# Performance work log

Measured on AMD Instinct MI355X. Metric: run time of the kernel, lower is better.

The kernel has to match this reference:

```python
import jax, jax.numpy as jnp
import numpy as np

B = 4096           # number of paths
N_STEPS = 4        # module hops per path (3 with tanh + final without)
E = 128            # embed_size
NUM_AUTHOR = 500000
NUM_MODULE = 64
OUT_DIM = 16       # classifier_output_dim


def setup_inputs() -> dict:
    key = jax.random.key(0)
    ks = jax.random.split(key, 7)
    author_ids = jax.random.randint(ks[0], (B,), 0, NUM_AUTHOR)
    module_ids = jax.random.randint(ks[1], (B, N_STEPS), 0, NUM_MODULE)
    # learned parameters (torch nn.Embedding / nn.Linear layout: W is [out, in])
    embed_table = jax.random.normal(ks[2], (NUM_AUTHOR, E), dtype=jnp.float32)
    W = jax.random.normal(ks[3], (NUM_MODULE, E, E), dtype=jnp.float32) * (1.0 / np.sqrt(E))
    b = jax.random.normal(ks[4], (NUM_MODULE, E), dtype=jnp.float32) * 0.01
    cls_W = jax.random.normal(ks[5], (OUT_DIM, E), dtype=jnp.float32) * (1.0 / np.sqrt(E))
    cls_b = jax.random.normal(ks[6], (OUT_DIM,), dtype=jnp.float32) * 0.01
    return {"author_ids": author_ids, "module_ids": module_ids,
            "embed_table": embed_table, "W": W, "b": b,
            "cls_W": cls_W, "cls_b": cls_b}


def reference(author_ids, module_ids, embed_table, W, b, cls_W, cls_b):
    # x = author embedding lookup (path[0])           [B, E]
    x = embed_table[author_ids]
    n_steps = module_ids.shape[1]
    # dynamically-selected Linear+tanh chain; final Linear has no tanh
    for i in range(n_steps):
        ids = module_ids[:, i]                        # [B]
        Wi = W[ids]                                   # [B, E, E] (out, in)
        bi = b[ids]                                   # [B, E]
        y = jnp.einsum('bi,boi->bo', x, Wi) + bi
        x = jnp.tanh(y) if i < n_steps - 1 else y
    # classifier: Linear(E -> OUT_DIM)
    return x @ cls_W.T + cls_b
```

## Files before the change

kernel.cpp:

```cpp
#include <hip/hip_runtime.h>

#define B_TOT   4096
#define NSTEPS  4
#define E       128
#define OUT_DIM 16
#define NMOD    64
#define KSPLIT  8
#define TILE    16

using frag8 = __attribute__((ext_vector_type(8))) short;
using f32x4 = __attribute__((ext_vector_type(4))) float;

__device__ __forceinline__ unsigned short f2bf(float x) {
    union { float f; unsigned u; } v; v.f = x;
    unsigned r = v.u + 0x7FFFu + ((v.u >> 16) & 1u);
    return (unsigned short)(r >> 16);
}
__device__ __forceinline__ float bf2f(unsigned short h) {
    union { unsigned u; float f; } v; v.u = ((unsigned)h) << 16;
    return v.f;
}
__device__ __forceinline__ unsigned pack2(unsigned short a, unsigned short b) {
    return (unsigned)a | ((unsigned)b << 16);
}
__device__ __forceinline__ float tanh_fast(float x) {
    return 1.0f - 2.0f / (__expf(2.0f * x) + 1.0f);
}


__global__ __launch_bounds__(1024) void sort_kernel(const int* __restrict__ mids,
                                                    int* __restrict__ ws)
{
    const int s = blockIdx.x;
    const int t = threadIdx.x;
    __shared__ int h[NMOD];
    __shared__ int o[NMOD];
    if (t < NMOD) h[t] = 0;
    __syncthreads();
    for (int b = t; b < B_TOT; b += 1024)
        atomicAdd(&h[mids[b * NSTEPS + s]], 1);
    __syncthreads();
    if (t == 0) {
        int run = 0;
        for (int m = 0; m < NMOD; ++m) { o[m] = run; run += h[m]; }
    }
    __syncthreads();
    if (t < NMOD) {
        ws[s * NMOD + t]       = h[t];
        ws[256 + s * NMOD + t] = o[t];
        h[t] = o[t];
    }
    __syncthreads();
    int* perm = ws + 512 + s * B_TOT;
    for (int b = t; b < B_TOT; b += 1024) {
        const int m = mids[b * NSTEPS + s];
        const int p = atomicAdd(&h[m], 1);
        perm[p] = b;
    }
}

template <bool FIRST, bool LAST>
__global__ __launch_bounds__(256) void step_kernel(
    const int s,
    const int* __restrict__ ws,
    const int* __restrict__ author_ids,
    const float* __restrict__ embed,
    const float* __restrict__ W,
    const float* __restrict__ bias,
    const float* __restrict__ cls_W,
    const float* __restrict__ cls_b,
    float* __restrict__ xbuf,
    float* __restrict__ out)
{
    const int m = blockIdx.x >> 3;
    const int k = blockIdx.x & (KSPLIT - 1);
    const int cnt = ws[s * NMOD + m];
    const int off = ws[256 + s * NMOD + m];
    const int start = off + k * TILE;
    const int end   = off + cnt;
    if (start >= end) return;

    const int t  = threadIdx.x;
    const int w  = t >> 6;
    const int l  = t & 63;
    const int g  = l >> 4;
    const int r0 = l & 15;

    __shared__ __align__(16) unsigned short Whi[E * E];
    __shared__ __align__(16) unsigned short Wlo[E * E];
    __shared__ __align__(16) unsigned short Xhi[TILE * E];
    __shared__ __align__(16) unsigned short Xlo[TILE * E];
    __shared__ __align__(16) float bl[E];
    __shared__ int rowb[TILE];
    __shared__ __align__(16) float YlS[LAST ? TILE * (E + 4) : 1];
    __shared__ __align__(16) float cwlS[LAST ? OUT_DIM * (E + 4) : 1];

    {
        const f32x4* __restrict__ wg = (const f32x4*)(W + (size_t)m * E * E);
        #pragma unroll
        for (int i = 0; i < 16; ++i) {
            const f32x4 v = wg[i * 256 + t];
            const int f  = (i * 256 + t) * 4;
            const int c  = f >> 7;
            const int kk = f & 127;
            const int idx = c * E + (((kk >> 3) ^ (c & 15)) << 3) + (kk & 7);
            const unsigned short h0 = f2bf(v.x), h1 = f2bf(v.y),
                                 h2 = f2bf(v.z), h3 = f2bf(v.w);
            const unsigned short q0 = f2bf(v.x - bf2f(h0)), q1 = f2bf(v.y - bf2f(h1)),
                                 q2 = f2bf(v.z - bf2f(h2)), q3 = f2bf(v.w - bf2f(h3));
            uint2 hp = { pack2(h0, h1), pack2(h2, h3) };
            uint2 lp = { pack2(q0, q1), pack2(q2, q3) };
            *(uint2*)&Whi[idx] = hp;
            *(uint2*)&Wlo[idx] = lp;
        }
        if (t < 32)
            ((f32x4*)bl)[t] = ((const f32x4*)(bias + m * E))[t];
        if (LAST) {
            #pragma unroll
            for (int i = 0; i < 2; ++i) {
                const int fi = i * 256 + t;
                const f32x4 v = ((const f32x4*)cls_W)[fi];
                const int j  = (fi * 4) >> 7;
                const int kk = (fi * 4) & 127;
                *(f32x4*)&cwlS[j * (E + 4) + kk] = v;
            }
        }
    }

    const int* __restrict__ perm = ws + 512 + s * B_TOT;
    const int c0 = 32 * w + r0;
    const int c1 = c0 + 16;

    for (int base = start; base < end; base += KSPLIT * TILE) {
        const int nb = min(TILE, end - base);

        {
            const int row = t >> 4, u0 = t & 15;
            f32x4 v0 = {0.f, 0.f, 0.f, 0.f}, v1 = {0.f, 0.f, 0.f, 0.f};
            if (row < nb) {
                const int b = perm[base + row];
                if (u0 == 0) rowb[row] = b;
                const float* __restrict__ src =
                    FIRST ? (embed + (size_t)author_ids[b] * E)
                          : (xbuf + (size_t)b * E);
                v0 = ((const f32x4*)src)[u0 * 2];
                v1 = ((const f32x4*)src)[u0 * 2 + 1];
            }
            const float xf[8] = {v0.x, v0.y, v0.z, v0.w, v1.x, v1.y, v1.z, v1.w};
            unsigned short hh[8], qq[8];
            #pragma unroll
            for (int j = 0; j < 8; ++j) {
                hh[j] = f2bf(xf[j]);
                qq[j] = f2bf(xf[j] - bf2f(hh[j]));
            }
            const int idx = row * E + ((u0 ^ row) << 3);
            uint4 hp = { pack2(hh[0], hh[1]), pack2(hh[2], hh[3]),
                         pack2(hh[4], hh[5]), pack2(hh[6], hh[7]) };
            uint4 lp = { pack2(qq[0], qq[1]), pack2(qq[2], qq[3]),
                         pack2(qq[4], qq[5]), pack2(qq[6], qq[7]) };
            *(uint4*)&Xhi[idx] = hp;
            *(uint4*)&Xlo[idx] = lp;
        }
        __syncthreads();

        frag8 ahi[4], alo[4];
        #pragma unroll
        for (int ss = 0; ss < 4; ++ss) {
            const int idx = r0 * E + (((4 * ss + g) ^ r0) << 3);
            ahi[ss] = *(const frag8*)&Xhi[idx];
            alo[ss] = *(const frag8*)&Xlo[idx];
        }

        f32x4 acc0 = {0.f, 0.f, 0.f, 0.f};
        f32x4 acc1 = {0.f, 0.f, 0.f, 0.f};
        #pragma unroll
        for (int ss = 0; ss < 4; ++ss) {
            const int u = ((4 * ss + g) ^ r0) << 3;
            {
                const int idx = c0 * E + u;
                const frag8 bh = *(const frag8*)&Whi[idx];
                const frag8 bq = *(const frag8*)&Wlo[idx];
                acc0 = __builtin_amdgcn_mfma_f32_16x16x32_bf16(ahi[ss], bh, acc0, 0, 0, 0);
                acc0 = __builtin_amdgcn_mfma_f32_16x16x32_bf16(alo[ss], bh, acc0, 0, 0, 0);
                acc0 = __builtin_amdgcn_mfma_f32_16x16x32_bf16(ahi[ss], bq, acc0, 0, 0, 0);
            }
            {
                const int idx = c1 * E + u;
                const frag8 bh = *(const frag8*)&Whi[idx];
                const frag8 bq = *(const frag8*)&Wlo[idx];
                acc1 = __builtin_amdgcn_mfma_f32_16x16x32_bf16(ahi[ss], bh, acc1, 0, 0, 0);
                acc1 = __builtin_amdgcn_mfma_f32_16x16x32_bf16(alo[ss], bh, acc1, 0, 0, 0);
                acc1 = __builtin_amdgcn_mfma_f32_16x16x32_bf16(ahi[ss], bq, acc1, 0, 0, 0);
            }
        }

        if (!LAST) {
            const float b0 = bl[c0], b1 = bl[c1];
            #pragma unroll
            for (int r = 0; r < 4; ++r) {
                const int row = 4 * g + r;
                if (row < nb) {
                    float* __restrict__ dst = xbuf + (size_t)rowb[row] * E;
                    dst[c0] = tanh_fast(acc0[r] + b0);
                    dst[c1] = tanh_fast(acc1[r] + b1);
                }
            }
            __syncthreads();
        } else {
            const float b0 = bl[c0], b1 = bl[c1];
            #pragma unroll
            for (int r = 0; r < 4; ++r) {
                const int row = 4 * g + r;
                YlS[row * (E + 4) + c0] = acc0[r] + b0;
                YlS[row * (E + 4) + c1] = acc1[r] + b1;
            }
            __syncthreads();
            const int row = t >> 4, j = t & 15;
            if (row < nb) {
                float a2 = cls_b[j];
                #pragma unroll 8
                for (int jj = 0; jj < 32; ++jj) {
                    const f32x4 y4 = *(const f32x4*)&YlS[row * (E + 4) + jj * 4];
                    const f32x4 w4 = *(const f32x4*)&cwlS[j * (E + 4) + jj * 4];
                    a2 += y4.x * w4.x + y4.y * w4.y + y4.z * w4.z + y4.w * w4.w;
                }
                out[(size_t)rowb[row] * OUT_DIM + j] = a2;
            }
            __syncthreads();
        }
    }
}

extern "C" void kernel_launch(void* const* d_in, const int* in_sizes, int n_in,
                              void* d_out, int out_size, void* d_ws, size_t ws_size,
                              hipStream_t stream) {
    const int*   author_ids = (const int*)d_in[0];
    const int*   module_ids = (const int*)d_in[1];
    const float* embed      = (const float*)d_in[2];
    const float* W          = (const float*)d_in[3];
    const float* bias       = (const float*)d_in[4];
    const float* cls_W      = (const float*)d_in[5];
    const float* cls_b      = (const float*)d_in[6];
    float* out = (float*)d_out;

    int*   wsI  = (int*)d_ws;
    float* xbuf = (float*)((char*)d_ws + (512 + NSTEPS * B_TOT) * sizeof(int));

    sort_kernel<<<NSTEPS, 1024, 0, stream>>>(module_ids, wsI);

    const dim3 g(NMOD * KSPLIT), blk(256);
    step_kernel<true,  false><<<g, blk, 0, stream>>>(0, wsI, author_ids, embed, W, bias, cls_W, cls_b, xbuf, out);
    step_kernel<false, false><<<g, blk, 0, stream>>>(1, wsI, author_ids, embed, W, bias, cls_W, cls_b, xbuf, out);
    step_kernel<false, false><<<g, blk, 0, stream>>>(2, wsI, author_ids, embed, W, bias, cls_W, cls_b, xbuf, out);
    step_kernel<false, true ><<<g, blk, 0, stream>>>(3, wsI, author_ids, embed, W, bias, cls_W, cls_b, xbuf, out);
}
```

Baseline: 48.14 us.

## Precompute bf16 hi/lo weight fragments once and drop LDS staging in step kernels

Result: slower. 50.14 us (+4.1%).

```diff
diff --git a/kernel.cpp b/kernel.cpp
--- a/kernel.cpp
+++ b/kernel.cpp
@@ -8,6 +8,9 @@
 #define KSPLIT  8
 #define TILE    16
 
+#define XBUF_BYTE  67584
+#define WFRAG_BYTE 2164736
+
 using frag8 = __attribute__((ext_vector_type(8))) short;
 using f32x4 = __attribute__((ext_vector_type(4))) float;
 
@@ -23,39 +26,71 @@
 __device__ __forceinline__ unsigned pack2(unsigned short a, unsigned short b) {
     return (unsigned)a | ((unsigned)b << 16);
 }
+__device__ __forceinline__ frag8 u4frag(uint4 u) {
+    union { uint4 u; frag8 f; } v; v.u = u; return v.f;
+}
 __device__ __forceinline__ float tanh_fast(float x) {
     return 1.0f - 2.0f / (__expf(2.0f * x) + 1.0f);
 }
 
-
-__global__ __launch_bounds__(1024) void sort_kernel(const int* __restrict__ mids,
-                                                    int* __restrict__ ws)
+__global__ __launch_bounds__(1024) void prep_sort_kernel(
+    const int* __restrict__ mids, const float* __restrict__ W, int* __restrict__ ws)
 {
-    const int s = blockIdx.x;
     const int t = threadIdx.x;
-    __shared__ int h[NMOD];
-    __shared__ int o[NMOD];
-    if (t < NMOD) h[t] = 0;
-    __syncthreads();
-    for (int b = t; b < B_TOT; b += 1024)
-        atomicAdd(&h[mids[b * NSTEPS + s]], 1);
-    __syncthreads();
-    if (t == 0) {
-        int run = 0;
-        for (int m = 0; m < NMOD; ++m) { o[m] = run; run += h[m]; }
-    }
-    __syncthreads();
-    if (t < NMOD) {
-        ws[s * NMOD + t]       = h[t];
-        ws[256 + s * NMOD + t] = o[t];
-        h[t] = o[t];
-    }
-    __syncthreads();
-    int* perm = ws + 512 + s * B_TOT;
-    for (int b = t; b < B_TOT; b += 1024) {
-        const int m = mids[b * NSTEPS + s];
-        const int p = atomicAdd(&h[m], 1);
-        perm[p] = b;
+    if (blockIdx.x < NSTEPS) {
+        const int s = blockIdx.x;
+        __shared__ int h[NMOD];
+        __shared__ int o[NMOD];
+        if (t < NMOD) h[t] = 0;
+        __syncthreads();
+        for (int b = t; b < B_TOT; b += 1024)
+            atomicAdd(&h[mids[b * NSTEPS + s]], 1);
+        __syncthreads();
+        if (t == 0) {
+            int run = 0;
+            for (int m = 0; m < NMOD; ++m) { o[m] = run; run += h[m]; }
+        }
+        __syncthreads();
+        if (t < NMOD) {
+            ws[s * NMOD + t]       = h[t];
+            ws[256 + s * NMOD + t] = o[t];
+            h[t] = o[t];
+        }
+        __syncthreads();
+        int* perm = ws + 512 + s * B_TOT;
+        for (int b = t; b < B_TOT; b += 1024) {
+            const int m = mids[b * NSTEPS + s];
+            const int p = atomicAdd(&h[m], 1);
+            perm[p] = b;
+        }
+    } else {
+        const int m = blockIdx.x - NSTEPS;
+        uint4* __restrict__ wf = (uint4*)((char*)ws + WFRAG_BYTE);
+        const f32x4* __restrict__ wg = (const f32x4*)(W + (size_t)m * E * E);
+        #pragma unroll
+        for (int i = 0; i < 2; ++i) {
+            const int f  = i * 1024 + t;
+            const int c  = f >> 4;
+            const int ss = (f >> 2) & 3;
+            const int g  = f & 3;
+            const int fi = (c * E + ss * 32 + g * 8) >> 2;
+            const f32x4 v0 = wg[fi];
+            const f32x4 v1 = wg[fi + 1];
+            const float xf[8] = {v0.x, v0.y, v0.z, v0.w, v1.x, v1.y, v1.z, v1.w};
+            unsigned short hh[8], qq[8];
+            #pragma unroll
+            for (int j = 0; j < 8; ++j) {
+                hh[j] = f2bf(xf[j]);
+                qq[j] = f2bf(xf[j] - bf2f(hh[j]));
+            }
+            const uint4 H = { pack2(hh[0], hh[1]), pack2(hh[2], hh[3]),
+                              pack2(hh[4], hh[5]), pack2(hh[6], hh[7]) };
+            const uint4 L = { pack2(qq[0], qq[1]), pack2(qq[2], qq[3]),
+                              pack2(qq[4], qq[5]), pack2(qq[6], qq[7]) };
+            const int u = m * 4096 + ss * 512 + c * 4 + g;
+            wf[u]        = H;
+            wf[u + 2048] = L;
+        }
     }
 }
 
@@ -65,11 +100,9 @@
     const int* __restrict__ ws,
     const int* __restrict__ author_ids,
     const float* __restrict__ embed,
-    const float* __restrict__ W,
     const float* __restrict__ bias,
     const float* __restrict__ cls_W,
     const float* __restrict__ cls_b,
-    float* __restrict__ xbuf,
     float* __restrict__ out)
 {
     const int m = blockIdx.x >> 3;
@@ -85,146 +118,106 @@
     const int l  = t & 63;
     const int g  = l >> 4;
     const int r0 = l & 15;
-
-    __shared__ __align__(16) unsigned short Whi[E * E];
-    __shared__ __align__(16) unsigned short Wlo[E * E];
-    __shared__ __align__(16) unsigned short Xhi[TILE * E];
-    __shared__ __align__(16) unsigned short Xlo[TILE * E];
-    __shared__ __align__(16) float bl[E];
-    __shared__ int rowb[TILE];
-    __shared__ __align__(16) float YlS[LAST ? TILE * (E + 4) : 1];
-    __shared__ __align__(16) float cwlS[LAST ? OUT_DIM * (E + 4) : 1];
-
-    {
-        const f32x4* __restrict__ wg = (const f32x4*)(W + (size_t)m * E * E);
-        #pragma unroll
-        for (int i = 0; i < 16; ++i) {
-            const f32x4 v = wg[i * 256 + t];
-            const int f  = (i * 256 + t) * 4;
-            const int c  = f >> 7;
-            const int kk = f & 127;
-            const int idx = c * E + (((kk >> 3) ^ (c & 15)) << 3) + (kk & 7);
-            const unsigned short h0 = f2bf(v.x), h1 = f2bf(v.y),
-                                 h2 = f2bf(v.z), h3 = f2bf(v.w);
-            const unsigned short q0 = f2bf(v.x - bf2f(h0)), q1 = f2bf(v.y - bf2f(h1)),
-                                 q2 = f2bf(v.z - bf2f(h2)), q3 = f2bf(v.w - bf2f(h3));
-            uint2 hp = { pack2(h0, h1), pack2(h2, h3) };
-            uint2 lp = { pack2(q0, q1), pack2(q2, q3) };
-            *(uint2*)&Whi[idx] = hp;
-            *(uint2*)&Wlo[idx] = lp;
-        }
-        if (t < 32)
-            ((f32x4*)bl)[t] = ((const f32x4*)(bias + m * E))[t];
-        if (LAST) {
-            #pragma unroll
-            for (int i = 0; i < 2; ++i) {
-                const int fi = i * 256 + t;
-                const f32x4 v = ((const f32x4*)cls_W)[fi];
-                const int j  = (fi * 4) >> 7;
-                const int kk = (fi * 4) & 127;
-                *(f32x4*)&cwlS[j * (E + 4) + kk] = v;
-            }
-        }
-    }
-
-    const int* __restrict__ perm = ws + 512 + s * B_TOT;
     const int c0 = 32 * w + r0;
     const int c1 = c0 + 16;
 
+    const int* __restrict__ perm = ws + 512 + s * B_TOT;
+    unsigned* __restrict__ xbufP = (unsigned*)((char*)ws + XBUF_BYTE);
+    const uint4* __restrict__ wf = (const uint4*)((char*)ws + WFRAG_BYTE) + m * 4096;
+
+    const float b0 = bias[m * E + c0];
+    const float b1 = bias[m * E + c1];
+
+    __shared__ __align__(16) float Yl[LAST ? TILE * (E + 4) : 1];
+
     for (int base = start; base < end; base += KSPLIT * TILE) {
         const int nb = min(TILE, end - base);
 
-        {
-            const int row = t >> 4, u0 = t & 15;
-            f32x4 v0 = {0.f, 0.f, 0.f, 0.f}, v1 = {0.f, 0.f, 0.f, 0.f};
-            if (row < nb) {
-                const int b = perm[base + row];
-                if (u0 == 0) rowb[row] = b;
-                const float* __restrict__ src =
-                    FIRST ? (embed + (size_t)author_ids[b] * E)
-                          : (xbuf + (size_t)b * E);
-                v0 = ((const f32x4*)src)[u0 * 2];
-                v1 = ((const f32x4*)src)[u0 * 2 + 1];
-            }
-            const float xf[8] = {v0.x, v0.y, v0.z, v0.w, v1.x, v1.y, v1.z, v1.w};
-            unsigned short hh[8], qq[8];
-            #pragma unroll
-            for (int j = 0; j < 8; ++j) {
-                hh[j] = f2bf(xf[j]);
-                qq[j] = f2bf(xf[j] - bf2f(hh[j]));
-            }
-            const int idx = row * E + ((u0 ^ row) << 3);
-            uint4 hp = { pack2(hh[0], hh[1]), pack2(hh[2], hh[3]),
-                         pack2(hh[4], hh[5]), pack2(hh[6], hh[7]) };
-            uint4 lp = { pack2(qq[0], qq[1]), pack2(qq[2], qq[3]),
-                         pack2(qq[4], qq[5]), pack2(qq[6], qq[7]) };
-            *(uint4*)&Xhi[idx] = hp;
-            *(uint4*)&Xlo[idx] = lp;
-        }
-        __syncthreads();
-
+        const bool rok = r0 < nb;
+        const int pa = perm[min(base + r0, B_TOT - 1)];
         frag8 ahi[4], alo[4];
-        #pragma unroll
-        for (int ss = 0; ss < 4; ++ss) {
-            const int idx = r0 * E + (((4 * ss + g) ^ r0) << 3);
-            ahi[ss] = *(const frag8*)&Xhi[idx];
-            alo[ss] = *(const frag8*)&Xlo[idx];
+        if (FIRST) {
+            const f32x4* __restrict__ src =
+                (const f32x4*)(embed + (size_t)author_ids[pa] * E);
+            #pragma unroll
+            for (int ss = 0; ss < 4; ++ss) {
+                f32x4 v0 = {0.f, 0.f, 0.f, 0.f}, v1 = {0.f, 0.f, 0.f, 0.f};
+                if (rok) { v0 = src[8 * ss + 2 * g]; v1 = src[8 * ss + 2 * g + 1]; }
+                const float xf[8] = {v0.x, v0.y, v0.z, v0.w, v1.x, v1.y, v1.z, v1.w};
+                #pragma unroll
+                for (int j = 0; j < 8; ++j) {
+                    const unsigned short hh = f2bf(xf[j]);
+                    ahi[ss][j] = (short)hh;
+                    alo[ss][j] = (short)f2bf(xf[j] - bf2f(hh));
+                }
+            }
+        } else {
+            const uint4* __restrict__ src = (const uint4*)(xbufP + (size_t)pa * E);
+            #pragma unroll
+            for (int ss = 0; ss < 4; ++ss) {
+                uint4 p0 = {0, 0, 0, 0}, p1 = {0, 0, 0, 0};
+                if (rok) { p0 = src[8 * ss + 2 * g]; p1 = src[8 * ss + 2 * g + 1]; }
+                const unsigned pv[8] = {p0.x, p0.y, p0.z, p0.w, p1.x, p1.y, p1.z, p1.w};
+                #pragma unroll
+                for (int j = 0; j < 8; ++j) {
+                    ahi[ss][j] = (short)(pv[j] >> 16);
+                    alo[ss][j] = (short)(pv[j] & 0xFFFFu);
+                }
+            }
         }
 
         f32x4 acc0 = {0.f, 0.f, 0.f, 0.f};
         f32x4 acc1 = {0.f, 0.f, 0.f, 0.f};
         #pragma unroll
         for (int ss = 0; ss < 4; ++ss) {
-            const int u = ((4 * ss + g) ^ r0) << 3;
-            {
-                const int idx = c0 * E + u;
-                const frag8 bh = *(const frag8*)&Whi[idx];
-                const frag8 bq = *(const frag8*)&Wlo[idx];
-                acc0 = __builtin_amdgcn_mfma_f32_16x16x32_bf16(ahi[ss], bh, acc0, 0, 0, 0);
-                acc0 = __builtin_amdgcn_mfma_f32_16x16x32_bf16(alo[ss], bh, acc0, 0, 0, 0);
-                acc0 = __builtin_amdgcn_mfma_f32_16x16x32_bf16(ahi[ss], bq, acc0, 0, 0, 0);
-            }
-            {
-                const int idx = c1 * E + u;
-                const frag8 bh = *(const frag8*)&Whi[idx];
-                const frag8 bq = *(const frag8*)&Wlo[idx];
-                acc1 = __builtin_amdgcn_mfma_f32_16x16x32_bf16(ahi[ss], bh, acc1, 0, 0, 0);
-                acc1 = __builtin_amdgcn_mfma_f32_16x16x32_bf16(alo[ss], bh, acc1, 0, 0, 0);
-                acc1 = __builtin_amdgcn_mfma_f32_16x16x32_bf16(ahi[ss], bq, acc1, 0, 0, 0);
-            }
+            const int u0 = ss * 512 + c0 * 4 + g;
+            const int u1 = ss * 512 + c1 * 4 + g;
+            const frag8 bh0 = u4frag(wf[u0]);
+            const frag8 bq0 = u4frag(wf[u0 + 2048]);
+            const frag8 bh1 = u4frag(wf[u1]);
+            const frag8 bq1 = u4frag(wf[u1 + 2048]);
+            acc0 = __builtin_amdgcn_mfma_f32_16x16x32_bf16(ahi[ss], bh0, acc0, 0, 0, 0);
+            acc0 = __builtin_amdgcn_mfma_f32_16x16x32_bf16(alo[ss], bh0, acc0, 0, 0, 0);
+            acc0 = __builtin_amdgcn_mfma_f32_16x16x32_bf16(ahi[ss], bq0, acc0, 0, 0, 0);
+            acc1 = __builtin_amdgcn_mfma_f32_16x16x32_bf16(ahi[ss], bh1, acc1, 0, 0, 0);
+            acc1 = __builtin_amdgcn_mfma_f32_16x16x32_bf16(alo[ss], bh1, acc1, 0, 0, 0);
+            acc1 = __builtin_amdgcn_mfma_f32_16x16x32_bf16(ahi[ss], bq1, acc1, 0, 0, 0);
         }
 
         if (!LAST) {
-            const float b0 = bl[c0], b1 = bl[c1];
             #pragma unroll
             for (int r = 0; r < 4; ++r) {
                 const int row = 4 * g + r;
                 if (row < nb) {
-                    float* __restrict__ dst = xbuf + (size_t)rowb[row] * E;
-                    dst[c0] = tanh_fast(acc0[r] + b0);
-                    dst[c1] = tanh_fast(acc1[r] + b1);
-                }
-            }
-            __syncthreads();
+                    const int rb = perm[base + row];
+                    const float y0 = tanh_fast(acc0[r] + b0);
+                    const float y1 = tanh_fast(acc1[r] + b1);
+                    const unsigned short h0 = f2bf(y0);
+                    const unsigned short h1 = f2bf(y1);
+                    unsigned* __restrict__ dst = xbufP + (size_t)rb * E;
+                    dst[c0] = pack2(f2bf(y0 - bf2f(h0)), h0);
+                    dst[c1] = pack2(f2bf(y1 - bf2f(h1)), h1);
+                }
+            }
         } else {
-            const float b0 = bl[c0], b1 = bl[c1];
             #pragma unroll
             for (int r = 0; r < 4; ++r) {
                 const int row = 4 * g + r;
-                YlS[row * (E + 4) + c0] = acc0[r] + b0;
-                YlS[row * (E + 4) + c1] = acc1[r] + b1;
+                Yl[row * (E + 4) + c0] = acc0[r] + b0;
+                Yl[row * (E + 4) + c1] = acc1[r] + b1;
             }
             __syncthreads();
             const int row = t >> 4, j = t & 15;
             if (row < nb) {
+                const f32x4* __restrict__ cw = (const f32x4*)(cls_W + j * E);
                 float a2 = cls_b[j];
                 #pragma unroll 8
                 for (int jj = 0; jj < 32; ++jj) {
-                    const f32x4 y4 = *(const f32x4*)&YlS[row * (E + 4) + jj * 4];
-                    const f32x4 w4 = *(const f32x4*)&cwlS[j * (E + 4) + jj * 4];
+                    const f32x4 y4 = *(const f32x4*)&Yl[row * (E + 4) + jj * 4];
+                    const f32x4 w4 = cw[jj];
                     a2 += y4.x * w4.x + y4.y * w4.y + y4.z * w4.z + y4.w * w4.w;
                 }
-                out[(size_t)rowb[row] * OUT_DIM + j] = a2;
+                out[(size_t)perm[base + row] * OUT_DIM + j] = a2;
             }
             __syncthreads();
         }
@@ -242,15 +235,13 @@
     const float* cls_W      = (const float*)d_in[5];
     const float* cls_b      = (const float*)d_in[6];
     float* out = (float*)d_out;
-
-    int*   wsI  = (int*)d_ws;
-    float* xbuf = (float*)((char*)d_ws + (512 + NSTEPS * B_TOT) * sizeof(int));
-
-    sort_kernel<<<NSTEPS, 1024, 0, stream>>>(module_ids, wsI);
+    int*   wsI = (int*)d_ws;
+
+    prep_sort_kernel<<<NSTEPS + NMOD, 1024, 0, stream>>>(module_ids, W, wsI);
 
     const dim3 g(NMOD * KSPLIT), blk(256);
-    step_kernel<true,  false><<<g, blk, 0, stream>>>(0, wsI, author_ids, embed, W, bias, cls_W, cls_b, xbuf, out);
-    step_kernel<false, false><<<g, blk, 0, stream>>>(1, wsI, author_ids, embed, W, bias, cls_W, cls_b, xbuf, out);
-    step_kernel<false, false><<<g, blk, 0, stream>>>(2, wsI, author_ids, embed, W, bias, cls_W, cls_b, xbuf, out);
-    step_kernel<false, true ><<<g, blk, 0, stream>>>(3, wsI, author_ids, embed, W, bias, cls_W, cls_b, xbuf, out);
-}
+    step_kernel<true,  false><<<g, blk, 0, stream>>>(0, wsI, author_ids, embed, bias, cls_W, cls_b, out);
+    step_kernel<false, false><<<g, blk, 0, stream>>>(1, wsI, author_ids, embed, bias, cls_W, cls_b, out);
+    step_kernel<false, false><<<g, blk, 0, stream>>>(2, wsI, author_ids, embed, bias, cls_W, cls_b, out);
+    step_kernel<false, true ><<<g, blk, 0, stream>>>(3, wsI, author_ids, embed, bias, cls_W, cls_b, out);
+}
```
